# Kernel tuning notes

Hardware: AMD Instinct MI355X
Metric: run time of the kernel (lower is better)

Reference implementation:

```python
import jax, jax.numpy as jnp
import numpy as np

NUM_HEADS = 16
HEAD_DIM = 64
ROPE_BASE = 160000.0


def _rope_tables(seq_len, head_dim):
    inv_freq = 1.0 / (ROPE_BASE ** (jnp.arange(0, head_dim, 2, dtype=jnp.float32) / head_dim))
    freqs = jnp.arange(seq_len, dtype=jnp.float32)[:, None] * inv_freq[None, :]  # [S, hd/2]
    return jnp.cos(freqs)[None, None], jnp.sin(freqs)[None, None]  # [1,1,S,hd/2]


def _apply_rope(x, cos, sin):
    # x: [B, nh, S, hd]; split-half rotation as in the torch module
    x1, x2 = jnp.split(x, 2, axis=-1)
    return jnp.concatenate([x1 * cos - x2 * sin, x2 * cos + x1 * sin], axis=-1)


def setup_inputs() -> dict:
    key = jax.random.key(0)
    k1, k2, k3 = jax.random.split(key, 3)
    B, S, H = 2, 2048, 1024
    hidden_states = jax.random.normal(k1, (B, S, H), dtype=jnp.float32)
    # additive causal mask: 0 for allowed, -1e9 for future positions
    causal = jnp.tril(jnp.ones((S, S), dtype=bool))
    attention_mask = jnp.where(causal, 0.0, -1e9).astype(jnp.float32)[None, None]
    Wqkv = jax.random.normal(k2, (H, 3 * H), dtype=jnp.float32) * (H ** -0.5)
    Wo = jax.random.normal(k3, (H, H), dtype=jnp.float32) * (H ** -0.5)
    return {"hidden_states": hidden_states, "attention_mask": attention_mask, "Wqkv": Wqkv, "Wo": Wo}


def reference(hidden_states, attention_mask, Wqkv, Wo):
    B, S, H = hidden_states.shape
    nh, hd = NUM_HEADS, HEAD_DIM
    scale = hd ** -0.5

    qkv = hidden_states @ Wqkv                                   # [B,S,3H]
    qkv = qkv.reshape(B, S, 3, nh, hd).transpose(2, 0, 3, 1, 4)  # [3,B,nh,S,hd]
    q, k, v = qkv[0], qkv[1], qkv[2]

    cos, sin = _rope_tables(S, hd)
    q = _apply_rope(q, cos, sin)
    k = _apply_rope(k, cos, sin)

    scores = jnp.einsum('bhqd,bhkd->bhqk', q, k) * scale + attention_mask
    attn = jax.nn.softmax(scores, axis=-1)
    out = jnp.einsum('bhqk,bhkd->bhqd', attn, v)                 # [B,nh,S,hd]
    out = out.transpose(0, 2, 1, 3).reshape(B, S, H)
    return out @ Wo
```

## Files before the change

### kernel.cpp

```cpp
#include <hip/hip_runtime.h>
#include <hip/hip_bf16.h>

typedef __bf16 bf16x8 __attribute__((ext_vector_type(8)));
typedef float f32x4 __attribute__((ext_vector_type(4)));
typedef unsigned short u16;

__device__ __forceinline__ u16 f2bf(float f) {
    union { float f; unsigned u; } x{f};
    unsigned r = x.u + 0x7fffu + ((x.u >> 16) & 1u);
    return (u16)(r >> 16);
}
__device__ __forceinline__ unsigned pk2(float a, float b) {
    union { float f; unsigned u; } x{a}, y{b};
    return ((x.u + 0x8000u) >> 16) | ((y.u + 0x8000u) & 0xffff0000u);
}
__device__ __forceinline__ float ex2(float x) { return __builtin_amdgcn_exp2f(x); }
__device__ __forceinline__ f32x4 zero4() { f32x4 z = {0.f, 0.f, 0.f, 0.f}; return z; }

typedef const __attribute__((address_space(1))) unsigned int* gp1_t;
typedef __attribute__((address_space(3))) unsigned int* lp3_t;
__device__ __forceinline__ void async16(const u16* g, u16* l) {
    __builtin_amdgcn_global_load_lds((gp1_t)g, (lp3_t)l, 16, 0, 0);
}

__global__ void __launch_bounds__(256) prep(const float* __restrict__ hs,
                                            u16* __restrict__ Xb,
                                            const float* __restrict__ Wqkv,
                                            u16* __restrict__ Wqkvt,
                                            const float* __restrict__ Wo,
                                            u16* __restrict__ Wot,
                                            float* __restrict__ cosT,
                                            float* __restrict__ sinT) {
    __shared__ float tile[32][33];
    const int blk = blockIdx.x, t = threadIdx.x;
    if (blk < 4096) {
        int i = (blk * 256 + t) * 4;
        float4 v = *(const float4*)(hs + i);
        ushort4 o;
        o.x = f2bf(v.x); o.y = f2bf(v.y); o.z = f2bf(v.z); o.w = f2bf(v.w);
        *(ushort4*)(Xb + i) = o;
    } else if (blk < 8192) {
        const float* W; u16* Wt; int N, bx, by;
        if (blk < 7168) { int bid = blk - 4096; W = Wqkv; Wt = Wqkvt; N = 3072; bx = bid % 96; by = bid / 96; }
        else            { int bid = blk - 7168; W = Wo;   Wt = Wot;   N = 1024; bx = bid % 32; by = bid / 32; }
        const int K = 1024;
        int tx = t & 31, ty = t >> 5;
        int n0 = bx * 32, k0 = by * 32;
#pragma unroll
        for (int i = 0; i < 32; i += 8)
            tile[ty + i][tx] = W[(size_t)(k0 + ty + i) * N + n0 + tx];
        __syncthreads();
#pragma unroll
        for (int i = 0; i < 32; i += 8)
            Wt[(size_t)(n0 + ty + i) * K + k0 + tx] = f2bf(tile[tx][ty + i]);
    } else {
        int idx = (blk - 8192) * 256 + t;
        int d = idx & 31, s = idx >> 5;
        float inv = expf(-(float)d * 0.374466538f);
        float th = (float)s * inv;
        cosT[idx] = cosf(th);
        sinT[idx] = sinf(th);
    }
}

__global__ void __launch_bounds__(256) vtrans(const u16* __restrict__ V,
                                              u16* __restrict__ Vt) {
    __shared__ u16 tile[32][33];
    int t = threadIdx.x;
    int tx = t & 31, ty = t >> 5;
    int s0 = blockIdx.x * 32, d0 = blockIdx.y * 32;
    size_t bi = (size_t)blockIdx.z * 2048 * 64;
#pragma unroll
    for (int i = 0; i < 32; i += 8)
        tile[ty + i][tx] = V[bi + (size_t)(s0 + ty + i) * 64 + d0 + tx];
    __syncthreads();
#pragma unroll
    for (int i = 0; i < 32; i += 8)
        Vt[bi + (size_t)(d0 + ty + i) * 2048 + s0 + tx] = tile[tx][ty + i];
}

__global__ void __launch_bounds__(256) gemm_qkv(const u16* __restrict__ A,
                                                const u16* __restrict__ Bt,
                                                const float* __restrict__ cosT,
                                                const float* __restrict__ sinT,
                                                u16* __restrict__ Q,
                                                u16* __restrict__ Kd,
                                                u16* __restrict__ V) {
    const int K = 1024, N = 3072;
    __shared__ __align__(16) u16 As[128 * 32];
    __shared__ __align__(16) u16 Bs[128 * 32];
    const int t = threadIdx.x;
    const int lane = t & 63, w = t >> 6;
    const int wm = w >> 1, wn = w & 1;
    const int m16 = lane & 15, q4 = lane >> 4;
    const int bm = blockIdx.y, bn = blockIdx.x;

    const int lrow = lane >> 2;
    const int kchunk = (lane & 3) ^ ((lane >> 3) & 3);
    const u16* Ag = A + (size_t)(bm * 128 + w * 32 + lrow) * K + kchunk * 8;
    const u16* Bg = Bt + (size_t)(bn * 128 + w * 32 + lrow) * K + kchunk * 8;
    u16* Al0 = As + (w * 32) * 32;
    u16* Al1 = As + (w * 32 + 16) * 32;
    u16* Bl0 = Bs + (w * 32) * 32;
    u16* Bl1 = Bs + (w * 32 + 16) * 32;
    const int kswz = (q4 ^ ((m16 >> 1) & 3)) * 8;

    f32x4 acc[4][4];
#pragma unroll
    for (int i = 0; i < 4; i++)
#pragma unroll
        for (int j = 0; j < 4; j++) acc[i][j] = zero4();

    for (int k0 = 0; k0 < K; k0 += 32) {
        __syncthreads();
        async16(Ag + k0, Al0);
        async16(Ag + 16 * K + k0, Al1);
        async16(Bg + k0, Bl0);
        async16(Bg + 16 * K + k0, Bl1);
        __syncthreads();
        bf16x8 af[4], bf[4];
#pragma unroll
        for (int i = 0; i < 4; i++)
            af[i] = *(const bf16x8*)&As[(wm * 64 + i * 16 + m16) * 32 + kswz];
#pragma unroll
        for (int j = 0; j < 4; j++)
            bf[j] = *(const bf16x8*)&Bs[(wn * 64 + j * 16 + m16) * 32 + kswz];
#pragma unroll
        for (int i = 0; i < 4; i++)
#pragma unroll
            for (int j = 0; j < 4; j++)
                acc[i][j] = __builtin_amdgcn_mfma_f32_16x16x32_bf16(af[i], bf[j], acc[i][j], 0, 0, 0);
    }

    const int colbase = bn * 128 + wn * 64;
    const int type = colbase >> 10;
    const int h = (colbase & 1023) >> 6;
    const int rbase = bm * 128 + wm * 64;

    if (type == 2) {
#pragma unroll
        for (int i = 0; i < 4; i++)
#pragma unroll
            for (int rr = 0; rr < 4; rr++) {
                int r = rbase + i * 16 + q4 * 4 + rr;
                int b = r >> 11, s = r & 2047;
                size_t ob = ((size_t)((b * 16 + h) * 2048 + s)) * 64;
#pragma unroll
                for (int j = 0; j < 4; j++)
                    V[ob + j * 16 + m16] = f2bf(acc[i][j][rr]);
            }
    } else {
        u16* dst = (type == 0) ? Q : Kd;
        const float qs = (type == 0) ? 0.1803368801f  : 1.0f;
#pragma unroll
        for (int i = 0; i < 4; i++)
#pragma unroll
            for (int rr = 0; rr < 4; rr++) {
                int r = rbase + i * 16 + q4 * 4 + rr;
                int b = r >> 11, s = r & 2047;
                size_t ob = ((size_t)((b * 16 + h) * 2048 + s)) * 64;
#pragma unroll
                for (int j2 = 0; j2 < 2; j2++) {
                    int d = j2 * 16 + m16;
                    float cs = cosT[s * 32 + d];
                    float sn = sinT[s * 32 + d];
                    float x1 = acc[i][j2][rr];
                    float x2 = acc[i][j2 + 2][rr];
                    dst[ob + d]      = f2bf((x1 * cs - x2 * sn) * qs);
                    dst[ob + d + 32] = f2bf((x2 * cs + x1 * sn) * qs);
                }
            }
    }
}

__global__ void __launch_bounds__(256) gemm_bt(const u16* __restrict__ A,
                                               const u16* __restrict__ Bt,
                                               float* __restrict__ C,
                                               int M, int N, int K) {
    __shared__ __align__(16) u16 As[128 * 32];
    __shared__ __align__(16) u16 Bs[128 * 32];
    const int t = threadIdx.x;
    const int lane = t & 63, w = t >> 6;
    const int wm = w >> 1, wn = w & 1;
    const int m16 = lane & 15, q4 = lane >> 4;
    const int bm = blockIdx.y, bn = blockIdx.x;

    const int lrow = lane >> 2;
    const int kchunk = (lane & 3) ^ ((lane >> 3) & 3);
    const u16* Ag = A + (size_t)(bm * 128 + w * 32 + lrow) * K + kchunk * 8;
    const u16* Bg = Bt + (size_t)(bn * 128 + w * 32 + lrow) * K + kchunk * 8;
    u16* Al0 = As + (w * 32) * 32;
    u16* Al1 = As + (w * 32 + 16) * 32;
    u16* Bl0 = Bs + (w * 32) * 32;
    u16* Bl1 = Bs + (w * 32 + 16) * 32;
    const int kswz = (q4 ^ ((m16 >> 1) & 3)) * 8;

    f32x4 acc[4][4];
#pragma unroll
    for (int i = 0; i < 4; i++)
#pragma unroll
        for (int j = 0; j < 4; j++) acc[i][j] = zero4();

    for (int k0 = 0; k0 < K; k0 += 32) {
        __syncthreads();
        async16(Ag + k0, Al0);
        async16(Ag + 16 * K + k0, Al1);
        async16(Bg + k0, Bl0);
        async16(Bg + 16 * K + k0, Bl1);
        __syncthreads();
        bf16x8 af[4], bf[4];
#pragma unroll
        for (int i = 0; i < 4; i++)
            af[i] = *(const bf16x8*)&As[(wm * 64 + i * 16 + m16) * 32 + kswz];
#pragma unroll
        for (int j = 0; j < 4; j++)
            bf[j] = *(const bf16x8*)&Bs[(wn * 64 + j * 16 + m16) * 32 + kswz];
#pragma unroll
        for (int i = 0; i < 4; i++)
#pragma unroll
            for (int j = 0; j < 4; j++)
                acc[i][j] = __builtin_amdgcn_mfma_f32_16x16x32_bf16(af[i], bf[j], acc[i][j], 0, 0, 0);
    }
#pragma unroll
    for (int i = 0; i < 4; i++)
#pragma unroll
        for (int j = 0; j < 4; j++)
#pragma unroll
            for (int rr = 0; rr < 4; rr++) {
                int row = bm * 128 + wm * 64 + i * 16 + q4 * 4 + rr;
                int col = bn * 128 + wn * 64 + j * 16 + m16;
                C[(size_t)row * N + col] = acc[i][j][rr];
            }
}

__global__ void __launch_bounds__(256) attn_kernel(const u16* __restrict__ Q,
                                                   const u16* __restrict__ Kg_,
                                                   const u16* __restrict__ Vtg_,
                                                   u16* __restrict__ O) {
    __shared__ __align__(16) u16 Ks[2][64][72];
    __shared__ __align__(16) u16 Vt[2][64][72];
    __shared__ __align__(16) u16 Pt[4][16][72];
    const int t = threadIdx.x, w = t >> 6;
    const int m16 = t & 15, q4 = (t & 63) >> 4;
    const int bx = blockIdx.x, bh = blockIdx.y;
    const size_t base = (size_t)bh * 2048 * 64;
    const int b = bh >> 4, h = bh & 15;
    const int skey = t >> 2, sc = (t & 3) * 16;

#pragma unroll 1
    for (int ph = 0; ph < 2; ph++) {
        const int qt = ph ? (31 - bx) : bx;
        const int qrow = qt * 64 + w * 16 + m16;
        const u16* Qg = Q + base + (size_t)qrow * 64;
        bf16x8 qf0 = *(const bf16x8*)(Qg + q4 * 8);
        bf16x8 qf1 = *(const bf16x8*)(Qg + 32 + q4 * 8);

        f32x4 occ[4];
#pragma unroll
        for (int dc = 0; dc < 4; dc++) occ[dc] = zero4();
        float li = 0.f;

        const u16* Kb0 = Kg_ + base + skey * 64 + sc;
        const u16* Vt0 = Vtg_ + base + (size_t)skey * 2048 + sc;
        uint4 ka = *(const uint4*)(Kb0);
        uint4 kb = *(const uint4*)(Kb0 + 8);
        uint4 va = *(const uint4*)(Vt0);
        uint4 vb = *(const uint4*)(Vt0 + 8);

#pragma unroll 1
        for (int jt = 0; jt <= qt; jt++) {
            const int bi = jt & 1;
            *(uint4*)&Ks[bi][skey][sc] = ka;
            *(uint4*)&Ks[bi][skey][sc + 8] = kb;
            *(uint4*)&Vt[bi][skey][sc] = va;
            *(uint4*)&Vt[bi][skey][sc + 8] = vb;
            if (jt < qt) {
                const u16* Kn = Kb0 + (size_t)(jt + 1) * 4096;
                const u16* Vn = Vt0 + (size_t)(jt + 1) * 64;
                ka = *(const uint4*)(Kn);
                kb = *(const uint4*)(Kn + 8);
                va = *(const uint4*)(Vn);
                vb = *(const uint4*)(Vn + 8);
            }
            __syncthreads();

            f32x4 st[4];
#pragma unroll
            for (int c = 0; c < 4; c++) st[c] = zero4();
#pragma unroll
            for (int c = 0; c < 4; c++) {
                bf16x8 kf0 = *(const bf16x8*)&Ks[bi][c * 16 + m16][q4 * 8];
                bf16x8 kf1 = *(const bf16x8*)&Ks[bi][c * 16 + m16][32 + q4 * 8];
                st[c] = __builtin_amdgcn_mfma_f32_16x16x32_bf16(kf0, qf0, st[c], 0, 0, 0);
                st[c] = __builtin_amdgcn_mfma_f32_16x16x32_bf16(kf1, qf1, st[c], 0, 0, 0);
            }

            float pv[4][4];
#pragma unroll
            for (int c = 0; c < 4; c++)
#pragma unroll
                for (int rr = 0; rr < 4; rr++) pv[c][rr] = st[c][rr];
            if (jt == qt) {
                const int ql = w * 16 + m16;
#pragma unroll
                for (int c = 0; c < 4; c++)
#pragma unroll
                    for (int rr = 0; rr < 4; rr++)
                        if (c * 16 + q4 * 4 + rr > ql) pv[c][rr] = -1e30f;
            }

#pragma unroll
            for (int c = 0; c < 4; c++) {
                float p0 = ex2(pv[c][0] - 24.f);
                float p1 = ex2(pv[c][1] - 24.f);
                float p2 = ex2(pv[c][2] - 24.f);
                float p3 = ex2(pv[c][3] - 24.f);
                li += (p0 + p1) + (p2 + p3);
                uint2 pkd = make_uint2(pk2(p0, p1), pk2(p2, p3));
                *(uint2*)&Pt[w][m16][c * 16 + q4 * 4] = pkd;
            }

#pragma unroll
            for (int ks = 0; ks < 2; ks++) {
                bf16x8 pf = *(const bf16x8*)&Pt[w][m16][ks * 32 + q4 * 8];
#pragma unroll
                for (int dc = 0; dc < 4; dc++) {
                    bf16x8 vf = *(const bf16x8*)&Vt[bi][dc * 16 + m16][ks * 32 + q4 * 8];
                    occ[dc] = __builtin_amdgcn_mfma_f32_16x16x32_bf16(vf, pf, occ[dc], 0, 0, 0);
                }
            }
        }

        li += __shfl_xor(li, 16);
        li += __shfl_xor(li, 32);
        float rli = 1.0f / li;
        u16* Op = O + ((size_t)(b * 2048 + qrow)) * 1024 + h * 64 + q4 * 4;
#pragma unroll
        for (int dc = 0; dc < 4; dc++) {
            ushort4 o;
            o.x = f2bf(occ[dc][0] * rli);
            o.y = f2bf(occ[dc][1] * rli);
            o.z = f2bf(occ[dc][2] * rli);
            o.w = f2bf(occ[dc][3] * rli);
            *(ushort4*)(Op + dc * 16) = o;
        }
        __syncthreads();
    }
}

extern "C" void kernel_launch(void* const* d_in, const int* in_sizes, int n_in,
                              void* d_out, int out_size, void* d_ws, size_t ws_size,
                              hipStream_t stream) {
    const float* hs   = (const float*)d_in[0];
    const float* Wqkv = (const float*)d_in[2];
    const float* Wo   = (const float*)d_in[3];
    float* out = (float*)d_out;

    const int BS = 4096;
    const int H = 1024, N3 = 3072;
    const int SH = 32 * 2048 * 64;

    u16* Xb    = (u16*)d_ws;
    u16* Wqkvt = Xb + (size_t)BS * H;
    u16* Wot   = Wqkvt + (size_t)N3 * H;
    u16* Qb    = Wot + (size_t)H * H;
    u16* Kb    = Qb + SH;
    u16* Vb    = Kb + SH;
    u16* Vtb   = Vb + SH;
    u16* AOb   = Vtb + SH;
    float* cosT = (float*)(AOb + (size_t)BS * H);
    float* sinT = cosT + 2048 * 32;

    prep<<<8448, 256, 0, stream>>>(hs, Xb, Wqkv, Wqkvt, Wo, Wot, cosT, sinT);

    gemm_qkv<<<dim3(N3 / 128, BS / 128), 256, 0, stream>>>(Xb, Wqkvt, cosT, sinT,
                                                           Qb, Kb, Vb);

    vtrans<<<dim3(64, 2, 32), 256, 0, stream>>>(Vb, Vtb);

    attn_kernel<<<dim3(16, 32), 256, 0, stream>>>(Qb, Kb, Vtb, AOb);

    gemm_bt<<<dim3(H / 128, BS / 128), 256, 0, stream>>>(AOb, Wot, out, BS, H, H);
}
```

Baseline: 210.9 us.

## Fuse V transpose into QKV GEMM epilogue and register-prefetch double-buffered GEMM loop

The QKV GEMM epilogue now writes V directly in transposed [d][s] layout with 4-element vector stores, which removes the separate vtrans kernel and its extra V buffer round trip. Both GEMMs now share a loop that prefetches the next K tile into registers and stores it into a double-buffered, padded LDS tile. This replaces the async global_load_lds path that had two barriers per iteration. The register-staged path uses more VGPRs and LDS and drops the XOR swizzle in favour of padding.

```diff
diff --git a/kernel.cpp b/kernel.cpp
--- a/kernel.cpp
+++ b/kernel.cpp
@@ -16,12 +16,6 @@
 }
 __device__ __forceinline__ float ex2(float x) { return __builtin_amdgcn_exp2f(x); }
 __device__ __forceinline__ f32x4 zero4() { f32x4 z = {0.f, 0.f, 0.f, 0.f}; return z; }
-
-typedef const __attribute__((address_space(1))) unsigned int* gp1_t;
-typedef __attribute__((address_space(3))) unsigned int* lp3_t;
-__device__ __forceinline__ void async16(const u16* g, u16* l) {
-    __builtin_amdgcn_global_load_lds((gp1_t)g, (lp3_t)l, 16, 0, 0);
-}
 
 __global__ void __launch_bounds__(256) prep(const float* __restrict__ hs,
                                             u16* __restrict__ Xb,
@@ -63,20 +57,58 @@
     }
 }
 
-__global__ void __launch_bounds__(256) vtrans(const u16* __restrict__ V,
-                                              u16* __restrict__ Vt) {
-    __shared__ u16 tile[32][33];
-    int t = threadIdx.x;
-    int tx = t & 31, ty = t >> 5;
-    int s0 = blockIdx.x * 32, d0 = blockIdx.y * 32;
-    size_t bi = (size_t)blockIdx.z * 2048 * 64;
-#pragma unroll
-    for (int i = 0; i < 32; i += 8)
-        tile[ty + i][tx] = V[bi + (size_t)(s0 + ty + i) * 64 + d0 + tx];
-    __syncthreads();
-#pragma unroll
-    for (int i = 0; i < 32; i += 8)
-        Vt[bi + (size_t)(d0 + ty + i) * 2048 + s0 + tx] = tile[tx][ty + i];
+struct GemmCtx {
+    f32x4 acc[4][4];
+    int m16, q4, wm, wn;
+};
+template <int KDIM>
+__device__ __forceinline__ void gemm_loop(const u16* __restrict__ A,
+                                          const u16* __restrict__ Bt,
+                                          int bm, int bn, GemmCtx& cx,
+                                          u16 (*As)[128][40], u16 (*Bs)[128][40]) {
+    const int t = threadIdx.x;
+    const int lane = t & 63, w = t >> 6;
+    cx.wm = w >> 1; cx.wn = w & 1;
+    cx.m16 = lane & 15; cx.q4 = lane >> 4;
+    const int r = t >> 1, c0 = (t & 1) * 16;
+
+    const u16* Ag = A + (size_t)(bm * 128 + r) * KDIM + c0;
+    const u16* Bg = Bt + (size_t)(bn * 128 + r) * KDIM + c0;
+
+#pragma unroll
+    for (int i = 0; i < 4; i++)
+#pragma unroll
+        for (int j = 0; j < 4; j++) cx.acc[i][j] = zero4();
+
+    uint4 a0 = *(const uint4*)(Ag);
+    uint4 a1 = *(const uint4*)(Ag + 8);
+    uint4 b0 = *(const uint4*)(Bg);
+    uint4 b1 = *(const uint4*)(Bg + 8);
+
+    for (int k0 = 0; k0 < KDIM; k0 += 32) {
+        const int bi = (k0 >> 5) & 1;
+        *(uint4*)&As[bi][r][c0] = a0; *(uint4*)&As[bi][r][c0 + 8] = a1;
+        *(uint4*)&Bs[bi][r][c0] = b0; *(uint4*)&Bs[bi][r][c0 + 8] = b1;
+        if (k0 + 32 < KDIM) {
+            a0 = *(const uint4*)(Ag + k0 + 32);
+            a1 = *(const uint4*)(Ag + k0 + 40);
+            b0 = *(const uint4*)(Bg + k0 + 32);
+            b1 = *(const uint4*)(Bg + k0 + 40);
+        }
+        __syncthreads();
+        bf16x8 af[4], bf[4];
+#pragma unroll
+        for (int i = 0; i < 4; i++)
+            af[i] = *(const bf16x8*)&As[bi][cx.wm * 64 + i * 16 + cx.m16][cx.q4 * 8];
+#pragma unroll
+        for (int j = 0; j < 4; j++)
+            bf[j] = *(const bf16x8*)&Bs[bi][cx.wn * 64 + j * 16 + cx.m16][cx.q4 * 8];
+#pragma unroll
+        for (int i = 0; i < 4; i++)
+#pragma unroll
+            for (int j = 0; j < 4; j++)
+                cx.acc[i][j] = __builtin_amdgcn_mfma_f32_16x16x32_bf16(af[i], bf[j], cx.acc[i][j], 0, 0, 0);
+    }
 }
 
 __global__ void __launch_bounds__(256) gemm_qkv(const u16* __restrict__ A,
@@ -85,59 +117,39 @@
                                                 const float* __restrict__ sinT,
                                                 u16* __restrict__ Q,
                                                 u16* __restrict__ Kd,
-                                                u16* __restrict__ V) {
-    const int K = 1024, N = 3072;
-    __shared__ __align__(16) u16 As[128 * 32];
-    __shared__ __align__(16) u16 Bs[128 * 32];
-    const int t = threadIdx.x;
-    const int lane = t & 63, w = t >> 6;
-    const int wm = w >> 1, wn = w & 1;
-    const int m16 = lane & 15, q4 = lane >> 4;
+                                                u16* __restrict__ Vt) {
+    __shared__ __align__(16) u16 As[2][128][40];
+    __shared__ __align__(16) u16 Bs[2][128][40];
+    GemmCtx cx;
     const int bm = blockIdx.y, bn = blockIdx.x;
-
-    const int lrow = lane >> 2;
-    const int kchunk = (lane & 3) ^ ((lane >> 3) & 3);
-    const u16* Ag = A + (size_t)(bm * 128 + w * 32 + lrow) * K + kchunk * 8;
-    const u16* Bg = Bt + (size_t)(bn * 128 + w * 32 + lrow) * K + kchunk * 8;
-    u16* Al0 = As + (w * 32) * 32;
-    u16* Al1 = As + (w * 32 + 16) * 32;
-    u16* Bl0 = Bs + (w * 32) * 32;
-    u16* Bl1 = Bs + (w * 32 + 16) * 32;
-    const int kswz = (q4 ^ ((m16 >> 1) & 3)) * 8;
-
-    f32x4 acc[4][4];
-#pragma unroll
-    for (int i = 0; i < 4; i++)
-#pragma unroll
-        for (int j = 0; j < 4; j++) acc[i][j] = zero4();
-
-    for (int k0 = 0; k0 < K; k0 += 32) {
-        __syncthreads();
-        async16(Ag + k0, Al0);
-        async16(Ag + 16 * K + k0, Al1);
-        async16(Bg + k0, Bl0);
-        async16(Bg + 16 * K + k0, Bl1);
-        __syncthreads();
-        bf16x8 af[4], bf[4];
-#pragma unroll
-        for (int i = 0; i < 4; i++)
-            af[i] = *(const bf16x8*)&As[(wm * 64 + i * 16 + m16) * 32 + kswz];
-#pragma unroll
-        for (int j = 0; j < 4; j++)
-            bf[j] = *(const bf16x8*)&Bs[(wn * 64 + j * 16 + m16) * 32 + kswz];
-#pragma unroll
-        for (int i = 0; i < 4; i++)
-#pragma unroll
-            for (int j = 0; j < 4; j++)
-                acc[i][j] = __builtin_amdgcn_mfma_f32_16x16x32_bf16(af[i], bf[j], acc[i][j], 0, 0, 0);
-    }
-
-    const int colbase = bn * 128 + wn * 64;
+    gemm_loop<1024>(A, Bt, bm, bn, cx, As, Bs);
+    const int m16 = cx.m16, q4 = cx.q4;
+
+    const int colbase = bn * 128 + cx.wn * 64;
     const int type = colbase >> 10;
     const int h = (colbase & 1023) >> 6;
-    const int rbase = bm * 128 + wm * 64;
+    const int rbase = bm * 128 + cx.wm * 64;
 
     if (type == 2) {
+#pragma unroll
+        for (int i = 0; i < 4; i++) {
+            int s0 = rbase + i * 16 + q4 * 4;
+            int b = s0 >> 11, sl = s0 & 2047;
+            size_t ob = (size_t)(b * 16 + h) * 64 * 2048;
+#pragma unroll
+            for (int j = 0; j < 4; j++) {
+                int d = j * 16 + m16;
+                ushort4 o;
+                o.x = f2bf(cx.acc[i][j][0]);
+                o.y = f2bf(cx.acc[i][j][1]);
+                o.z = f2bf(cx.acc[i][j][2]);
+                o.w = f2bf(cx.acc[i][j][3]);
+                *(ushort4*)&Vt[ob + (size_t)d * 2048 + sl] = o;
+            }
+        }
+    } else {
+        u16* dst = (type == 0) ? Q : Kd;
+        const float qs = (type == 0) ? 0.1803368801f  : 1.0f;
 #pragma unroll
         for (int i = 0; i < 4; i++)
 #pragma unroll
@@ -146,26 +158,12 @@
                 int b = r >> 11, s = r & 2047;
                 size_t ob = ((size_t)((b * 16 + h) * 2048 + s)) * 64;
 #pragma unroll
-                for (int j = 0; j < 4; j++)
-                    V[ob + j * 16 + m16] = f2bf(acc[i][j][rr]);
-            }
-    } else {
-        u16* dst = (type == 0) ? Q : Kd;
-        const float qs = (type == 0) ? 0.1803368801f  : 1.0f;
-#pragma unroll
-        for (int i = 0; i < 4; i++)
-#pragma unroll
-            for (int rr = 0; rr < 4; rr++) {
-                int r = rbase + i * 16 + q4 * 4 + rr;
-                int b = r >> 11, s = r & 2047;
-                size_t ob = ((size_t)((b * 16 + h) * 2048 + s)) * 64;
-#pragma unroll
                 for (int j2 = 0; j2 < 2; j2++) {
                     int d = j2 * 16 + m16;
                     float cs = cosT[s * 32 + d];
                     float sn = sinT[s * 32 + d];
-                    float x1 = acc[i][j2][rr];
-                    float x2 = acc[i][j2 + 2][rr];
+                    float x1 = cx.acc[i][j2][rr];
+                    float x2 = cx.acc[i][j2 + 2][rr];
                     dst[ob + d]      = f2bf((x1 * cs - x2 * sn) * qs);
                     dst[ob + d + 32] = f2bf((x2 * cs + x1 * sn) * qs);
                 }
@@ -173,63 +171,24 @@
     }
 }
 
-__global__ void __launch_bounds__(256) gemm_bt(const u16* __restrict__ A,
-                                               const u16* __restrict__ Bt,
-                                               float* __restrict__ C,
-                                               int M, int N, int K) {
-    __shared__ __align__(16) u16 As[128 * 32];
-    __shared__ __align__(16) u16 Bs[128 * 32];
-    const int t = threadIdx.x;
-    const int lane = t & 63, w = t >> 6;
-    const int wm = w >> 1, wn = w & 1;
-    const int m16 = lane & 15, q4 = lane >> 4;
+__global__ void __launch_bounds__(256) gemm_out(const u16* __restrict__ A,
+                                                const u16* __restrict__ Bt,
+                                                float* __restrict__ C) {
+    __shared__ __align__(16) u16 As[2][128][40];
+    __shared__ __align__(16) u16 Bs[2][128][40];
+    GemmCtx cx;
     const int bm = blockIdx.y, bn = blockIdx.x;
-
-    const int lrow = lane >> 2;
-    const int kchunk = (lane & 3) ^ ((lane >> 3) & 3);
-    const u16* Ag = A + (size_t)(bm * 128 + w * 32 + lrow) * K + kchunk * 8;
-    const u16* Bg = Bt + (size_t)(bn * 128 + w * 32 + lrow) * K + kchunk * 8;
-    u16* Al0 = As + (w * 32) * 32;
-    u16* Al1 = As + (w * 32 + 16) * 32;
-    u16* Bl0 = Bs + (w * 32) * 32;
-    u16* Bl1 = Bs + (w * 32 + 16) * 32;
-    const int kswz = (q4 ^ ((m16 >> 1) & 3)) * 8;
-
-    f32x4 acc[4][4];
+    gemm_loop<1024>(A, Bt, bm, bn, cx, As, Bs);
+    const int N = 1024;
 #pragma unroll
     for (int i = 0; i < 4; i++)
 #pragma unroll
-        for (int j = 0; j < 4; j++) acc[i][j] = zero4();
-
-    for (int k0 = 0; k0 < K; k0 += 32) {
-        __syncthreads();
-        async16(Ag + k0, Al0);
-        async16(Ag + 16 * K + k0, Al1);
-        async16(Bg + k0, Bl0);
-        async16(Bg + 16 * K + k0, Bl1);
-        __syncthreads();
-        bf16x8 af[4], bf[4];
-#pragma unroll
-        for (int i = 0; i < 4; i++)
-            af[i] = *(const bf16x8*)&As[(wm * 64 + i * 16 + m16) * 32 + kswz];
-#pragma unroll
         for (int j = 0; j < 4; j++)
-            bf[j] = *(const bf16x8*)&Bs[(wn * 64 + j * 16 + m16) * 32 + kswz];
-#pragma unroll
-        for (int i = 0; i < 4; i++)
-#pragma unroll
-            for (int j = 0; j < 4; j++)
-                acc[i][j] = __builtin_amdgcn_mfma_f32_16x16x32_bf16(af[i], bf[j], acc[i][j], 0, 0, 0);
-    }
-#pragma unroll
-    for (int i = 0; i < 4; i++)
-#pragma unroll
-        for (int j = 0; j < 4; j++)
 #pragma unroll
             for (int rr = 0; rr < 4; rr++) {
-                int row = bm * 128 + wm * 64 + i * 16 + q4 * 4 + rr;
-                int col = bn * 128 + wn * 64 + j * 16 + m16;
-                C[(size_t)row * N + col] = acc[i][j][rr];
+                int row = bm * 128 + cx.wm * 64 + i * 16 + cx.q4 * 4 + rr;
+                int col = bn * 128 + cx.wn * 64 + j * 16 + cx.m16;
+                C[(size_t)row * N + col] = cx.acc[i][j][rr];
             }
 }
 
@@ -365,8 +324,7 @@
     u16* Wot   = Wqkvt + (size_t)N3 * H;
     u16* Qb    = Wot + (size_t)H * H;
     u16* Kb    = Qb + SH;
-    u16* Vb    = Kb + SH;
-    u16* Vtb   = Vb + SH;
+    u16* Vtb   = Kb + SH;
     u16* AOb   = Vtb + SH;
     float* cosT = (float*)(AOb + (size_t)BS * H);
     float* sinT = cosT + 2048 * 32;
@@ -374,11 +332,9 @@
     prep<<<8448, 256, 0, stream>>>(hs, Xb, Wqkv, Wqkvt, Wo, Wot, cosT, sinT);
 
     gemm_qkv<<<dim3(N3 / 128, BS / 128), 256, 0, stream>>>(Xb, Wqkvt, cosT, sinT,
-                                                           Qb, Kb, Vb);
-
-    vtrans<<<dim3(64, 2, 32), 256, 0, stream>>>(Vb, Vtb);
+                                                           Qb, Kb, Vtb);
 
     attn_kernel<<<dim3(16, 32), 256, 0, stream>>>(Qb, Kb, Vtb, AOb);
 
-    gemm_bt<<<dim3(H / 128, BS / 128), 256, 0, stream>>>(AOb, Wot, out, BS, H, H);
-}
+    gemm_out<<<dim3(H / 128, BS / 128), 256, 0, stream>>>(AOb, Wot, out);
+}
```

Measured after the change: 201.1 us. -4.7%, faster.
